# Optimization experiments

Measured on AMD Instinct MI355X. Metric: run time of the kernel, lower is better.

The kernel has to match this reference:

```python
import jax, jax.numpy as jnp
import numpy as np

N = 50000      # nodes
E = 800000     # edges (avg degree 16)
D = 128        # in_channels == hidden_channels (required by x*M + x_hat*~M)
OUT = 64       # fc out_channels


def _linear_params(key, out_f, in_f):
    # torch.nn.Linear default init: U(-1/sqrt(in), 1/sqrt(in))
    bound = 1.0 / np.sqrt(in_f)
    kw, kb = jax.random.split(key)
    W = jax.random.uniform(kw, (out_f, in_f), jnp.float32, -bound, bound)
    b = jax.random.uniform(kb, (out_f,), jnp.float32, -bound, bound)
    return W, b


def setup_inputs() -> dict:
    key = jax.random.key(0)
    ks = jax.random.split(key, 8)
    x = jax.random.normal(ks[0], (N, D), jnp.float32)
    edge_index = jax.random.randint(ks[1], (2, E), 0, N, dtype=jnp.int64)
    edge_weight = jax.random.uniform(ks[2], (E,), jnp.float32)
    M = jax.random.randint(ks[3], (N, D), 0, 2) > 0  # bool mask
    W1, b1 = _linear_params(ks[4], D, D)
    W2, b2 = _linear_params(ks[5], D, D)
    W3, b3 = _linear_params(ks[6], D, D)
    Wf, bf = _linear_params(ks[7], OUT, D)
    # extra Parameter `bias` in each FPLayer is zero-initialized
    z = jnp.zeros((D,), jnp.float32)
    return {"edge_index": edge_index, "edge_weight": edge_weight, "x": x, "M": M,
            "W1": W1, "b1": b1, "bias1": z, "W2": W2, "b2": b2, "bias2": z,
            "W3": W3, "b3": b3, "bias3": z, "Wf": Wf, "bf": bf}


def reference(edge_index, edge_weight, x, M,
              W1, b1, bias1, W2, b2, bias2, W3, b3, bias3, Wf, bf):
    row, col = edge_index[0], edge_index[1]
    n = x.shape[0]
    # symmetric degree normalization based on destination-node in-degree
    deg = jax.ops.segment_sum(jnp.ones(row.shape[0], x.dtype), col, num_segments=n)
    safe = jnp.where(deg > 0, deg, 1.0)
    dinv = jnp.where(deg > 0, 1.0 / jnp.sqrt(safe), 0.0)
    norm = dinv[row] * dinv[col]  # [E]  (edge_weight is unused by message())

    def fp_layer(x_tilde, W, b, bias):
        msg = norm[:, None] * x_tilde[row]                      # [E, D] gather
        agg = jax.ops.segment_sum(msg, col, num_segments=n)     # [N, D] scatter-add
        return agg @ W.T + b + bias

    # conv1: x_hat = 0 -> x_tilde = x*M
    h = jax.nn.relu(fp_layer(jnp.where(M, x, 0.0), W1, b1, bias1))
    h = jax.nn.relu(fp_layer(jnp.where(M, x, h), W2, b2, bias2))
    h = jax.nn.relu(fp_layer(jnp.where(M, x, h), W3, b3, bias3))
    return h @ Wf.T + bf
```

## Files before the change

### kernel.cpp

```cpp
#include <hip/hip_runtime.h>

#define DD 128
#define OUTF 64
#define SCAP 64
#define NBUCK 8
#define PB_CAP 224
#define CHB 96

typedef __attribute__((ext_vector_type(8))) _Float16 fp16x8;
typedef __attribute__((ext_vector_type(8))) unsigned short ushort8;
typedef __attribute__((ext_vector_type(4))) float floatx4;

union h16 { _Float16 f; unsigned short u; };

__global__ __launch_bounds__(256) void setup_kernel(
    const int* __restrict__ ei, unsigned long long* __restrict__ pairbuf,
    int* __restrict__ pcnt, int* __restrict__ cursor, int E, int n,
    const float* __restrict__ x, const void* __restrict__ M,
    _Float16* __restrict__ xsel, int nd4,
    const float* __restrict__ W1, const float* __restrict__ W2,
    const float* __restrict__ W3, const float* __restrict__ Wf,
    _Float16* __restrict__ Bh1, _Float16* __restrict__ Bl1,
    _Float16* __restrict__ Bh2, _Float16* __restrict__ Bl2,
    _Float16* __restrict__ Bh3, _Float16* __restrict__ Bl3,
    _Float16* __restrict__ Bhf, _Float16* __restrict__ Blf,
    int nbA, int nbXt) {
    int bid = blockIdx.x;
    int t = threadIdx.x;
    if (bid < nbA) {
        __shared__ int lcnt[NBUCK];
        __shared__ int s_any;
        for (int z = bid * 256 + t; z < n; z += nbA * 256) cursor[z] = 0;
        if (t < NBUCK) lcnt[t] = 0;
        if (t == 0) s_any = 0;
        __syncthreads();
        int e0 = bid * 1024;
        int es = min(e0 + t * 4, E - 1);
        if (ei[2 * es + 1] != 0) s_any = 1;
        __syncthreads();
        bool is64 = (s_any == 0);
        float binv = (float)NBUCK / (float)n;
        for (int j = 0; j < 4; j++) {
            int e = e0 + j * 256 + t;
            if (e < E) {
                int r, c;
                if (is64) {
                    const long long* p = (const long long*)ei;
                    r = (int)p[e];
                    c = (int)p[(size_t)E + e];
                } else {
                    r = ei[e];
                    c = ei[E + e];
                }
                r = min(max(r, 0), n - 1);
                c = min(max(c, 0), n - 1);
                int b = min(NBUCK - 1, (int)((float)c * binv));
                int pos = atomicAdd(&lcnt[b], 1);
                if (pos < PB_CAP)
                    pairbuf[((size_t)bid * NBUCK + b) * PB_CAP + pos] =
                        ((unsigned long long)(unsigned)c << 32) | (unsigned)r;
            }
        }
        __syncthreads();
        if (t < NBUCK) pcnt[bid * NBUCK + t] = min(lcnt[t], PB_CAP);
    } else if (bid < nbA + nbXt) {
        __shared__ int s_u8;
        if (t == 0) s_u8 = 0;
        __syncthreads();
        int i40 = (bid - nbA) * 256;
        size_t nd = (size_t)nd4 * 4;
        size_t ps = (size_t)i40 * 4 + (size_t)t * 4 + 1;
        if (ps >= nd) ps = nd - 1;
        if (((const unsigned char*)M)[ps] != 0) s_u8 = 1;
        __syncthreads();
        int isU8 = s_u8;
        int i4 = i40 + t;
        if (i4 < nd4) {
            size_t base = (size_t)i4 * 4;
            const float4 xv = *(const float4*)&x[base];
            int m0, m1, m2, m3;
            if (isU8) {
                const unsigned char* mp = (const unsigned char*)M + base;
                m0 = mp[0]; m1 = mp[1]; m2 = mp[2]; m3 = mp[3];
            } else {
                const int* mp = (const int*)M + base;
                m0 = mp[0]; m1 = mp[1]; m2 = mp[2]; m3 = mp[3];
            }
            h16 h0, h1, h2, h3;
            h0.f = (_Float16)xv.x; h1.f = (_Float16)xv.y;
            h2.f = (_Float16)xv.z; h3.f = (_Float16)xv.w;
            unsigned short s0 = m0 ? h0.u : (unsigned short)0xFFFF;
            unsigned short s1 = m1 ? h1.u : (unsigned short)0xFFFF;
            unsigned short s2 = m2 ? h2.u : (unsigned short)0xFFFF;
            unsigned short s3 = m3 ? h3.u : (unsigned short)0xFFFF;
            unsigned long long pk = (unsigned long long)s0 | ((unsigned long long)s1 << 16)
                                  | ((unsigned long long)s2 << 32) | ((unsigned long long)s3 << 48);
            *(unsigned long long*)&xsel[base] = pk;
        }
    } else {
        int tid = (bid - nbA - nbXt) * 256 + t;
        const float* W; _Float16 *Bh, *Bl; int NT, lt;
        if      (tid < 2048) { W = W1; Bh = Bh1; Bl = Bl1; NT = 8; lt = tid; }
        else if (tid < 4096) { W = W2; Bh = Bh2; Bl = Bl2; NT = 8; lt = tid - 2048; }
        else if (tid < 6144) { W = W3; Bh = Bh3; Bl = Bl3; NT = 8; lt = tid - 4096; }
        else if (tid < 7168) { W = Wf; Bh = Bhf; Bl = Blf; NT = 4; lt = tid - 6144; }
        else return;
        int lane = lt & 63;
        int g = lt >> 6;
        int nt = g % NT;
        int chunk = g / NT;
        int o = nt * 16 + (lane & 15);
        int k = chunk * 32 + (lane >> 4) * 8;
        const float* src = W + o * 128 + k;
#pragma unroll
        for (int j = 0; j < 8; j++) {
            float a = src[j];
            _Float16 h = (_Float16)a;
            Bh[(size_t)lt * 8 + j] = h;
            Bl[(size_t)lt * 8 + j] = (_Float16)(a - (float)h);
        }
    }
}

__global__ __launch_bounds__(256) void scatter_kernel(
    const unsigned long long* __restrict__ pairbuf,
    const int* __restrict__ pcnt,
    int* __restrict__ cursor, int* __restrict__ slot, int nbA) {
    int b = blockIdx.x & (NBUCK - 1);
    int chunk = blockIdx.x >> 3;
    int t = threadIdx.x;
    for (int i = chunk; i < nbA; i += CHB) {
        int cnt = pcnt[i * NBUCK + b];
        const unsigned long long* pp = pairbuf + ((size_t)i * NBUCK + b) * PB_CAP;
        for (int j = t; j < cnt; j += 256) {
            unsigned long long pr = pp[j];
            int c = (int)(pr >> 32);
            int r = (int)(unsigned)pr;
            int pos = atomicAdd(&cursor[c], 1);
            if (pos < SCAP)
                slot[(size_t)c * SCAP + pos] = r;
        }
    }
}

template <int SENT>
__global__ __launch_bounds__(256) void agg_kernel(const _Float16* __restrict__ xin,
                                                  const int* __restrict__ cursor,
                                                  const int* __restrict__ slot,
                                                  _Float16* __restrict__ A, int n) {
    int wave = (blockIdx.x * 256 + threadIdx.x) >> 6;
    if (wave >= n) return;
    int lane = threadIdx.x & 63;
    int sid = lane >> 4;
    int li = lane & 15;
    int craw = cursor[wave];
    int cnt = min(craw, SCAP);
    float dc = craw > 0 ? rsqrtf((float)craw) : 0.0f;
    const int* sl = slot + (size_t)wave * SCAP;
    float acc[8] = {0.f, 0.f, 0.f, 0.f, 0.f, 0.f, 0.f, 0.f};
    for (int k = 0; k < cnt; k += 16) {
        int i0 = k + sid;
        int i1 = k + 4 + sid;
        int i2 = k + 8 + sid;
        int i3 = k + 12 + sid;
        int r0 = sl[min(i0, cnt - 1)];
        int r1 = sl[min(i1, cnt - 1)];
        int r2 = sl[min(i2, cnt - 1)];
        int r3 = sl[min(i3, cnt - 1)];
        int c0 = cursor[r0], c1 = cursor[r1], c2 = cursor[r2], c3 = cursor[r3];
        float w0 = (i0 < cnt && c0 > 0) ? dc * rsqrtf((float)c0) : 0.0f;
        float w1 = (i1 < cnt && c1 > 0) ? dc * rsqrtf((float)c1) : 0.0f;
        float w2 = (i2 < cnt && c2 > 0) ? dc * rsqrtf((float)c2) : 0.0f;
        float w3 = (i3 < cnt && c3 > 0) ? dc * rsqrtf((float)c3) : 0.0f;
        ushort8 u0 = *(const ushort8*)&xin[(size_t)r0 * DD + li * 8];
        ushort8 u1 = *(const ushort8*)&xin[(size_t)r1 * DD + li * 8];
        ushort8 u2 = *(const ushort8*)&xin[(size_t)r2 * DD + li * 8];
        ushort8 u3 = *(const ushort8*)&xin[(size_t)r3 * DD + li * 8];
#pragma unroll
        for (int j = 0; j < 8; j++) {
            h16 t0, t1, t2, t3;
            if (SENT) {
                t0.u = (u0[j] == (unsigned short)0xFFFF) ? (unsigned short)0 : u0[j];
                t1.u = (u1[j] == (unsigned short)0xFFFF) ? (unsigned short)0 : u1[j];
                t2.u = (u2[j] == (unsigned short)0xFFFF) ? (unsigned short)0 : u2[j];
                t3.u = (u3[j] == (unsigned short)0xFFFF) ? (unsigned short)0 : u3[j];
            } else {
                t0.u = u0[j]; t1.u = u1[j]; t2.u = u2[j]; t3.u = u3[j];
            }
            acc[j] += w0 * (float)t0.f + w1 * (float)t1.f
                    + w2 * (float)t2.f + w3 * (float)t3.f;
        }
    }
#pragma unroll
    for (int j = 0; j < 8; j++) {
        acc[j] += __shfl_xor(acc[j], 16);
        acc[j] += __shfl_xor(acc[j], 32);
    }
    if (sid == 0) {
        fp16x8 o;
#pragma unroll
        for (int j = 0; j < 8; j++) o[j] = (_Float16)acc[j];
        *(fp16x8*)&A[(size_t)wave * DD + li * 8] = o;
    }
}

template <int MODE>
__global__ __launch_bounds__(256) void gemm_mfma(const _Float16* __restrict__ A,
                                                 const _Float16* __restrict__ Bh,
                                                 const _Float16* __restrict__ Bl,
                                                 const float* __restrict__ b,
                                                 const float* __restrict__ bias,
                                                 const _Float16* __restrict__ B2h,
                                                 const _Float16* __restrict__ B2l,
                                                 const float* __restrict__ b2,
                                                 float* __restrict__ out_f,
                                                 const _Float16* __restrict__ xsel,
                                                 _Float16* __restrict__ xt_out,
                                                 int n) {
    __shared__ __align__(16) _Float16 sh[4][16][136];
    int wid = (blockIdx.x * 256 + threadIdx.x) >> 6;
    int nwaves = n >> 4;
    if (wid >= nwaves) return;
    int n0 = wid * 16;
    int lane = threadIdx.x & 63;
    int li = lane & 15;
    int quad = lane >> 4;
    int wv = (threadIdx.x >> 6) & 3;

    floatx4 acc[8];
#pragma unroll
    for (int nt = 0; nt < 8; nt++)
        acc[nt] = (floatx4){0.f, 0.f, 0.f, 0.f};

    const _Float16* arow = A + (size_t)(n0 + li) * DD + quad * 8;
#pragma unroll
    for (int chunk = 0; chunk < 4; chunk++) {
        fp16x8 a = *(const fp16x8*)(arow + chunk * 32);
#pragma unroll
        for (int nt = 0; nt < 8; nt++) {
            size_t boff = (size_t)(((chunk * 8 + nt) << 6) + lane) * 8;
            fp16x8 b_h = *(const fp16x8*)&Bh[boff];
            fp16x8 b_l = *(const fp16x8*)&Bl[boff];
            acc[nt] = __builtin_amdgcn_mfma_f32_16x16x32_f16(a, b_h, acc[nt], 0, 0, 0);
            acc[nt] = __builtin_amdgcn_mfma_f32_16x16x32_f16(a, b_l, acc[nt], 0, 0, 0);
        }
    }

#pragma unroll
    for (int nt = 0; nt < 8; nt++) {
        int o = nt * 16 + li;
        float bb = b[o] + bias[o];
#pragma unroll
        for (int reg = 0; reg < 4; reg++) {
            float v = fmaxf(acc[nt][reg] + bb, 0.0f);
            sh[wv][quad * 4 + reg][o] = (_Float16)v;
        }
    }
    __asm__ volatile("s_waitcnt lgkmcnt(0)" ::: "memory");

    if (MODE == 0) {
#pragma unroll
        for (int it = 0; it < 4; it++) {
            int node = it * 4 + quad;
            size_t ix = (size_t)(n0 + node) * DD + li * 8;
            fp16x8 hv = *(const fp16x8*)&sh[wv][node][li * 8];
            fp16x8 xv = *(const fp16x8*)&xsel[ix];
            ushort8 xb = *(const ushort8*)&xsel[ix];
            fp16x8 o;
#pragma unroll
            for (int j = 0; j < 8; j++)
                o[j] = (xb[j] == (unsigned short)0xFFFF) ? hv[j] : xv[j];
            *(fp16x8*)&xt_out[ix] = o;
        }
    } else {
        floatx4 acc2[4];
#pragma unroll
        for (int nt = 0; nt < 4; nt++)
            acc2[nt] = (floatx4){0.f, 0.f, 0.f, 0.f};
#pragma unroll
        for (int chunk = 0; chunk < 4; chunk++) {
            fp16x8 a2 = *(const fp16x8*)&sh[wv][li][chunk * 32 + quad * 8];
#pragma unroll
            for (int nt = 0; nt < 4; nt++) {
                size_t boff = (size_t)(((chunk * 4 + nt) << 6) + lane) * 8;
                fp16x8 b_h = *(const fp16x8*)&B2h[boff];
                fp16x8 b_l = *(const fp16x8*)&B2l[boff];
                acc2[nt] = __builtin_amdgcn_mfma_f32_16x16x32_f16(a2, b_h, acc2[nt], 0, 0, 0);
                acc2[nt] = __builtin_amdgcn_mfma_f32_16x16x32_f16(a2, b_l, acc2[nt], 0, 0, 0);
            }
        }
        __asm__ volatile("s_waitcnt lgkmcnt(0)" ::: "memory");
        float* shf = (float*)&sh[wv][0][0];
#pragma unroll
        for (int nt = 0; nt < 4; nt++) {
            int o = nt * 16 + li;
            float bb = b2[o];
#pragma unroll
            for (int reg = 0; reg < 4; reg++)
                shf[(quad * 4 + reg) * 68 + o] = acc2[nt][reg] + bb;
        }
        __asm__ volatile("s_waitcnt lgkmcnt(0)" ::: "memory");
#pragma unroll
        for (int it = 0; it < 4; it++) {
            int node = it * 4 + quad;
            float4 v = *(const float4*)&shf[node * 68 + li * 4];
            *(float4*)&out_f[(size_t)(n0 + node) * OUTF + li * 4] = v;
        }
    }
}

extern "C" void kernel_launch(void* const* d_in, const int* in_sizes, int n_in,
                              void* d_out, int out_size, void* d_ws, size_t ws_size,
                              hipStream_t stream) {
    const int*   ei    = (const int*)d_in[0];
    const float* x     = (const float*)d_in[2];
    const void*  M     = d_in[3];
    const float* W1    = (const float*)d_in[4];
    const float* b1    = (const float*)d_in[5];
    const float* bias1 = (const float*)d_in[6];
    const float* W2    = (const float*)d_in[7];
    const float* b2    = (const float*)d_in[8];
    const float* bias2 = (const float*)d_in[9];
    const float* W3    = (const float*)d_in[10];
    const float* b3    = (const float*)d_in[11];
    const float* bias3 = (const float*)d_in[12];
    const float* Wf    = (const float*)d_in[13];
    const float* bf    = (const float*)d_in[14];

    const int E = in_sizes[1];
    const int N = in_sizes[2] / DD;
    const int ND = N * DD;

    char* w = (char*)d_ws;
    size_t off = 0;
    auto alloc = [&](size_t bytes) -> char* {
        char* p = w + off;
        off = (off + bytes + 255) & ~(size_t)255;
        return p;
    };
    const int nbA = (E + 1023) / 1024;
    int*   cursor = (int*)  alloc((size_t)N * 4);
    int*   slot   = (int*)  alloc((size_t)N * SCAP * 4);
    unsigned long long* pairbuf =
        (unsigned long long*)alloc((size_t)nbA * NBUCK * PB_CAP * 8);
    int*   pcnt   = (int*)  alloc((size_t)nbA * NBUCK * 4);
    _Float16* xsel = (_Float16*)alloc((size_t)ND * 2);
    _Float16* xt   = (_Float16*)alloc((size_t)ND * 2);
    _Float16* Aa   = (_Float16*)alloc((size_t)ND * 2);
    _Float16* Bh1 = (_Float16*)alloc(128 * 128 * 2);
    _Float16* Bl1 = (_Float16*)alloc(128 * 128 * 2);
    _Float16* Bh2 = (_Float16*)alloc(128 * 128 * 2);
    _Float16* Bl2 = (_Float16*)alloc(128 * 128 * 2);
    _Float16* Bh3 = (_Float16*)alloc(128 * 128 * 2);
    _Float16* Bl3 = (_Float16*)alloc(128 * 128 * 2);
    _Float16* Bhf = (_Float16*)alloc(64 * 128 * 2);
    _Float16* Blf = (_Float16*)alloc(64 * 128 * 2);
    (void)ws_size;

    const int nd4 = ND / 4;
    const int nbXt = (nd4 + 255) / 256;
    const int nbPk = 28;

    setup_kernel<<<nbA + nbXt + nbPk, 256, 0, stream>>>(
        ei, pairbuf, pcnt, cursor, E, N,
        x, M, xsel, nd4,
        W1, W2, W3, Wf,
        Bh1, Bl1, Bh2, Bl2, Bh3, Bl3, Bhf, Blf,
        nbA, nbXt);
    scatter_kernel<<<NBUCK * CHB, 256, 0, stream>>>(pairbuf, pcnt, cursor, slot, nbA);

    int nwaves = N / 16;
    int gGrid = (nwaves * 64 + 255) / 256;
    int aggGrid = (N * 64 + 255) / 256;

    agg_kernel<1><<<aggGrid, 256, 0, stream>>>(xsel, cursor, slot, Aa, N);
    gemm_mfma<0><<<gGrid, 256, 0, stream>>>(Aa, Bh1, Bl1, b1, bias1,
                                            nullptr, nullptr, nullptr, nullptr,
                                            xsel, xt, N);
    agg_kernel<0><<<aggGrid, 256, 0, stream>>>(xt, cursor, slot, Aa, N);
    gemm_mfma<0><<<gGrid, 256, 0, stream>>>(Aa, Bh2, Bl2, b2, bias2,
                                            nullptr, nullptr, nullptr, nullptr,
                                            xsel, xt, N);
    agg_kernel<0><<<aggGrid, 256, 0, stream>>>(xt, cursor, slot, Aa, N);
    gemm_mfma<1><<<gGrid, 256, 0, stream>>>(Aa, Bh3, Bl3, b3, bias3,
                                            Bhf, Blf, bf, (float*)d_out,
                                            nullptr, nullptr, N);
}
```

Measured before the change: 292.4 us.

## Prescale node features by source dinv and drop per-edge degree lookups

The symmetric normalization is factored so each node's features are pre-multiplied by its own dinv, both when the masked input is built and in the GEMM epilogue. Aggregation then sums unweighted neighbor rows and applies the destination dinv once, which removes the per-edge cursor gather and rsqrt. The x/M packing moves from the setup kernel into the scatter kernel, and those blocks spin on an atomic counter until the scatter blocks have finished computing degrees. The spin-wait depends on all scatter blocks being resident or scheduled ahead of the waiting blocks, and the prescaling slightly changes where fp16 rounding occurs.

```diff
diff --git a/kernel.cpp b/kernel.cpp
--- a/kernel.cpp
+++ b/kernel.cpp
@@ -6,6 +6,7 @@
 #define NBUCK 8
 #define PB_CAP 224
 #define CHB 96
+#define SCATB (NBUCK * CHB)
 
 typedef __attribute__((ext_vector_type(8))) _Float16 fp16x8;
 typedef __attribute__((ext_vector_type(8))) unsigned short ushort8;
@@ -15,21 +16,21 @@
 
 __global__ __launch_bounds__(256) void setup_kernel(
     const int* __restrict__ ei, unsigned long long* __restrict__ pairbuf,
-    int* __restrict__ pcnt, int* __restrict__ cursor, int E, int n,
-    const float* __restrict__ x, const void* __restrict__ M,
-    _Float16* __restrict__ xsel, int nd4,
+    int* __restrict__ pcnt, int* __restrict__ cursor, int* __restrict__ ctrl,
+    int E, int n,
     const float* __restrict__ W1, const float* __restrict__ W2,
     const float* __restrict__ W3, const float* __restrict__ Wf,
     _Float16* __restrict__ Bh1, _Float16* __restrict__ Bl1,
     _Float16* __restrict__ Bh2, _Float16* __restrict__ Bl2,
     _Float16* __restrict__ Bh3, _Float16* __restrict__ Bl3,
     _Float16* __restrict__ Bhf, _Float16* __restrict__ Blf,
-    int nbA, int nbXt) {
+    int nbA) {
     int bid = blockIdx.x;
     int t = threadIdx.x;
     if (bid < nbA) {
         __shared__ int lcnt[NBUCK];
         __shared__ int s_any;
+        if (bid == 0 && t == 0) ctrl[0] = 0;
         for (int z = bid * 256 + t; z < n; z += nbA * 256) cursor[z] = 0;
         if (t < NBUCK) lcnt[t] = 0;
         if (t == 0) s_any = 0;
@@ -63,42 +64,8 @@
         }
         __syncthreads();
         if (t < NBUCK) pcnt[bid * NBUCK + t] = min(lcnt[t], PB_CAP);
-    } else if (bid < nbA + nbXt) {
-        __shared__ int s_u8;
-        if (t == 0) s_u8 = 0;
-        __syncthreads();
-        int i40 = (bid - nbA) * 256;
-        size_t nd = (size_t)nd4 * 4;
-        size_t ps = (size_t)i40 * 4 + (size_t)t * 4 + 1;
-        if (ps >= nd) ps = nd - 1;
-        if (((const unsigned char*)M)[ps] != 0) s_u8 = 1;
-        __syncthreads();
-        int isU8 = s_u8;
-        int i4 = i40 + t;
-        if (i4 < nd4) {
-            size_t base = (size_t)i4 * 4;
-            const float4 xv = *(const float4*)&x[base];
-            int m0, m1, m2, m3;
-            if (isU8) {
-                const unsigned char* mp = (const unsigned char*)M + base;
-                m0 = mp[0]; m1 = mp[1]; m2 = mp[2]; m3 = mp[3];
-            } else {
-                const int* mp = (const int*)M + base;
-                m0 = mp[0]; m1 = mp[1]; m2 = mp[2]; m3 = mp[3];
-            }
-            h16 h0, h1, h2, h3;
-            h0.f = (_Float16)xv.x; h1.f = (_Float16)xv.y;
-            h2.f = (_Float16)xv.z; h3.f = (_Float16)xv.w;
-            unsigned short s0 = m0 ? h0.u : (unsigned short)0xFFFF;
-            unsigned short s1 = m1 ? h1.u : (unsigned short)0xFFFF;
-            unsigned short s2 = m2 ? h2.u : (unsigned short)0xFFFF;
-            unsigned short s3 = m3 ? h3.u : (unsigned short)0xFFFF;
-            unsigned long long pk = (unsigned long long)s0 | ((unsigned long long)s1 << 16)
-                                  | ((unsigned long long)s2 << 32) | ((unsigned long long)s3 << 48);
-            *(unsigned long long*)&xsel[base] = pk;
-        }
     } else {
-        int tid = (bid - nbA - nbXt) * 256 + t;
+        int tid = (bid - nbA) * 256 + t;
         const float* W; _Float16 *Bh, *Bl; int NT, lt;
         if      (tid < 2048) { W = W1; Bh = Bh1; Bl = Bl1; NT = 8; lt = tid; }
         else if (tid < 4096) { W = W2; Bh = Bh2; Bl = Bl2; NT = 8; lt = tid - 2048; }
@@ -125,20 +92,78 @@
 __global__ __launch_bounds__(256) void scatter_kernel(
     const unsigned long long* __restrict__ pairbuf,
     const int* __restrict__ pcnt,
-    int* __restrict__ cursor, int* __restrict__ slot, int nbA) {
-    int b = blockIdx.x & (NBUCK - 1);
-    int chunk = blockIdx.x >> 3;
+    int* __restrict__ cursor, int* __restrict__ slot, int* __restrict__ ctrl,
+    const float* __restrict__ x, const void* __restrict__ Mv,
+    _Float16* __restrict__ xs0, float* __restrict__ dinv,
+    int nbA, int ndTot) {
+    int bid = blockIdx.x;
     int t = threadIdx.x;
-    for (int i = chunk; i < nbA; i += CHB) {
-        int cnt = pcnt[i * NBUCK + b];
-        const unsigned long long* pp = pairbuf + ((size_t)i * NBUCK + b) * PB_CAP;
-        for (int j = t; j < cnt; j += 256) {
-            unsigned long long pr = pp[j];
-            int c = (int)(pr >> 32);
-            int r = (int)(unsigned)pr;
-            int pos = atomicAdd(&cursor[c], 1);
-            if (pos < SCAP)
-                slot[(size_t)c * SCAP + pos] = r;
+    if (bid < SCATB) {
+        int b = bid & (NBUCK - 1);
+        int chunk = bid >> 3;
+        for (int i = chunk; i < nbA; i += CHB) {
+            int cnt = pcnt[i * NBUCK + b];
+            const unsigned long long* pp = pairbuf + ((size_t)i * NBUCK + b) * PB_CAP;
+            for (int j = t; j < cnt; j += 256) {
+                unsigned long long pr = pp[j];
+                int c = (int)(pr >> 32);
+                int r = (int)(unsigned)pr;
+                int pos = atomicAdd(&cursor[c], 1);
+                if (pos < SCAP)
+                    slot[(size_t)c * SCAP + pos] = r;
+            }
+        }
+        __syncthreads();
+        __threadfence();
+        if (t == 0)
+            __hip_atomic_fetch_add(ctrl, 1, __ATOMIC_RELEASE, __HIP_MEMORY_SCOPE_AGENT);
+    } else {
+        size_t idx = (size_t)(bid - SCATB) * 2048 + (size_t)t * 8;
+        bool act = (idx + 8 <= (size_t)ndTot);
+        float4 xa = {0.f, 0.f, 0.f, 0.f}, xb = {0.f, 0.f, 0.f, 0.f};
+        if (act) {
+            xa = *(const float4*)&x[idx];
+            xb = *(const float4*)&x[idx + 4];
+        }
+        __shared__ int s_u8;
+        if (t == 0) s_u8 = 0;
+        __syncthreads();
+        size_t ps = idx + 1;
+        if (ps >= (size_t)ndTot) ps = (size_t)ndTot - 1;
+        if (((const unsigned char*)Mv)[ps] != 0) s_u8 = 1;
+        __syncthreads();
+        int m[8] = {0, 0, 0, 0, 0, 0, 0, 0};
+        if (act) {
+            if (s_u8) {
+                const unsigned char* mp = (const unsigned char*)Mv + idx;
+#pragma unroll
+                for (int j = 0; j < 8; j++) m[j] = mp[j];
+            } else {
+                const int* mp = (const int*)Mv + idx;
+#pragma unroll
+                for (int j = 0; j < 8; j++) m[j] = mp[j];
+            }
+        }
+        if (t == 0) {
+            while (__hip_atomic_load(ctrl, __ATOMIC_ACQUIRE, __HIP_MEMORY_SCOPE_AGENT) < SCATB)
+                __builtin_amdgcn_s_sleep(2);
+        }
+        __syncthreads();
+        if (act) {
+            int node = (int)(idx >> 7);
+            int deg = __hip_atomic_load(&cursor[node], __ATOMIC_RELAXED,
+                                        __HIP_MEMORY_SCOPE_AGENT);
+            float dv = deg > 0 ? rsqrtf((float)deg) : 0.0f;
+            if ((idx & 127) == 0) dinv[node] = dv;
+            float xf[8] = {xa.x, xa.y, xa.z, xa.w, xb.x, xb.y, xb.z, xb.w};
+            ushort8 o;
+#pragma unroll
+            for (int j = 0; j < 8; j++) {
+                h16 h;
+                h.f = (_Float16)(dv * xf[j]);
+                o[j] = m[j] ? h.u : (unsigned short)0xFFFF;
+            }
+            *(ushort8*)&xs0[idx] = o;
         }
     }
 }
@@ -147,15 +172,15 @@
 __global__ __launch_bounds__(256) void agg_kernel(const _Float16* __restrict__ xin,
                                                   const int* __restrict__ cursor,
                                                   const int* __restrict__ slot,
+                                                  const float* __restrict__ dinv,
                                                   _Float16* __restrict__ A, int n) {
     int wave = (blockIdx.x * 256 + threadIdx.x) >> 6;
     if (wave >= n) return;
     int lane = threadIdx.x & 63;
     int sid = lane >> 4;
     int li = lane & 15;
-    int craw = cursor[wave];
-    int cnt = min(craw, SCAP);
-    float dc = craw > 0 ? rsqrtf((float)craw) : 0.0f;
+    int cnt = min(cursor[wave], SCAP);
+    float dc = dinv[wave];
     const int* sl = slot + (size_t)wave * SCAP;
     float acc[8] = {0.f, 0.f, 0.f, 0.f, 0.f, 0.f, 0.f, 0.f};
     for (int k = 0; k < cnt; k += 16) {
@@ -167,28 +192,35 @@
         int r1 = sl[min(i1, cnt - 1)];
         int r2 = sl[min(i2, cnt - 1)];
         int r3 = sl[min(i3, cnt - 1)];
-        int c0 = cursor[r0], c1 = cursor[r1], c2 = cursor[r2], c3 = cursor[r3];
-        float w0 = (i0 < cnt && c0 > 0) ? dc * rsqrtf((float)c0) : 0.0f;
-        float w1 = (i1 < cnt && c1 > 0) ? dc * rsqrtf((float)c1) : 0.0f;
-        float w2 = (i2 < cnt && c2 > 0) ? dc * rsqrtf((float)c2) : 0.0f;
-        float w3 = (i3 < cnt && c3 > 0) ? dc * rsqrtf((float)c3) : 0.0f;
-        ushort8 u0 = *(const ushort8*)&xin[(size_t)r0 * DD + li * 8];
-        ushort8 u1 = *(const ushort8*)&xin[(size_t)r1 * DD + li * 8];
-        ushort8 u2 = *(const ushort8*)&xin[(size_t)r2 * DD + li * 8];
-        ushort8 u3 = *(const ushort8*)&xin[(size_t)r3 * DD + li * 8];
-#pragma unroll
-        for (int j = 0; j < 8; j++) {
-            h16 t0, t1, t2, t3;
-            if (SENT) {
+        float m0 = i0 < cnt ? 1.0f : 0.0f;
+        float m1 = i1 < cnt ? 1.0f : 0.0f;
+        float m2 = i2 < cnt ? 1.0f : 0.0f;
+        float m3 = i3 < cnt ? 1.0f : 0.0f;
+        if (SENT) {
+            ushort8 u0 = *(const ushort8*)&xin[(size_t)r0 * DD + li * 8];
+            ushort8 u1 = *(const ushort8*)&xin[(size_t)r1 * DD + li * 8];
+            ushort8 u2 = *(const ushort8*)&xin[(size_t)r2 * DD + li * 8];
+            ushort8 u3 = *(const ushort8*)&xin[(size_t)r3 * DD + li * 8];
+#pragma unroll
+            for (int j = 0; j < 8; j++) {
+                h16 t0, t1, t2, t3;
                 t0.u = (u0[j] == (unsigned short)0xFFFF) ? (unsigned short)0 : u0[j];
                 t1.u = (u1[j] == (unsigned short)0xFFFF) ? (unsigned short)0 : u1[j];
                 t2.u = (u2[j] == (unsigned short)0xFFFF) ? (unsigned short)0 : u2[j];
                 t3.u = (u3[j] == (unsigned short)0xFFFF) ? (unsigned short)0 : u3[j];
-            } else {
-                t0.u = u0[j]; t1.u = u1[j]; t2.u = u2[j]; t3.u = u3[j];
-            }
-            acc[j] += w0 * (float)t0.f + w1 * (float)t1.f
-                    + w2 * (float)t2.f + w3 * (float)t3.f;
+                acc[j] += m0 * (float)t0.f + m1 * (float)t1.f
+                        + m2 * (float)t2.f + m3 * (float)t3.f;
+            }
+        } else {
+            fp16x8 v0 = *(const fp16x8*)&xin[(size_t)r0 * DD + li * 8];
+            fp16x8 v1 = *(const fp16x8*)&xin[(size_t)r1 * DD + li * 8];
+            fp16x8 v2 = *(const fp16x8*)&xin[(size_t)r2 * DD + li * 8];
+            fp16x8 v3 = *(const fp16x8*)&xin[(size_t)r3 * DD + li * 8];
+#pragma unroll
+            for (int j = 0; j < 8; j++) {
+                acc[j] += m0 * (float)v0[j] + m1 * (float)v1[j]
+                        + m2 * (float)v2[j] + m3 * (float)v3[j];
+            }
         }
     }
 #pragma unroll
@@ -199,7 +231,7 @@
     if (sid == 0) {
         fp16x8 o;
 #pragma unroll
-        for (int j = 0; j < 8; j++) o[j] = (_Float16)acc[j];
+        for (int j = 0; j < 8; j++) o[j] = (_Float16)(dc * acc[j]);
         *(fp16x8*)&A[(size_t)wave * DD + li * 8] = o;
     }
 }
@@ -210,11 +242,12 @@
                                                  const _Float16* __restrict__ Bl,
                                                  const float* __restrict__ b,
                                                  const float* __restrict__ bias,
+                                                 const float* __restrict__ dinv,
                                                  const _Float16* __restrict__ B2h,
                                                  const _Float16* __restrict__ B2l,
                                                  const float* __restrict__ b2,
                                                  float* __restrict__ out_f,
-                                                 const _Float16* __restrict__ xsel,
+                                                 const _Float16* __restrict__ xs0,
                                                  _Float16* __restrict__ xt_out,
                                                  int n) {
     __shared__ __align__(16) _Float16 sh[4][16][136];
@@ -246,6 +279,11 @@
         }
     }
 
+    float dvr[4] = {1.f, 1.f, 1.f, 1.f};
+    if (MODE == 0) {
+        float4 dv4 = *(const float4*)&dinv[n0 + quad * 4];
+        dvr[0] = dv4.x; dvr[1] = dv4.y; dvr[2] = dv4.z; dvr[3] = dv4.w;
+    }
 #pragma unroll
     for (int nt = 0; nt < 8; nt++) {
         int o = nt * 16 + li;
@@ -253,6 +291,7 @@
 #pragma unroll
         for (int reg = 0; reg < 4; reg++) {
             float v = fmaxf(acc[nt][reg] + bb, 0.0f);
+            if (MODE == 0) v *= dvr[reg];
             sh[wv][quad * 4 + reg][o] = (_Float16)v;
         }
     }
@@ -264,8 +303,8 @@
             int node = it * 4 + quad;
             size_t ix = (size_t)(n0 + node) * DD + li * 8;
             fp16x8 hv = *(const fp16x8*)&sh[wv][node][li * 8];
-            fp16x8 xv = *(const fp16x8*)&xsel[ix];
-            ushort8 xb = *(const ushort8*)&xsel[ix];
+            fp16x8 xv = *(const fp16x8*)&xs0[ix];
+            ushort8 xb = *(const ushort8*)&xs0[ix];
             fp16x8 o;
 #pragma unroll
             for (int j = 0; j < 8; j++)
@@ -339,12 +378,14 @@
         return p;
     };
     const int nbA = (E + 1023) / 1024;
+    int*   ctrl   = (int*)  alloc(256);
     int*   cursor = (int*)  alloc((size_t)N * 4);
     int*   slot   = (int*)  alloc((size_t)N * SCAP * 4);
+    float* dinv   = (float*)alloc((size_t)N * 4);
     unsigned long long* pairbuf =
         (unsigned long long*)alloc((size_t)nbA * NBUCK * PB_CAP * 8);
     int*   pcnt   = (int*)  alloc((size_t)nbA * NBUCK * 4);
-    _Float16* xsel = (_Float16*)alloc((size_t)ND * 2);
+    _Float16* xs0  = (_Float16*)alloc((size_t)ND * 2);
     _Float16* xt   = (_Float16*)alloc((size_t)ND * 2);
     _Float16* Aa   = (_Float16*)alloc((size_t)ND * 2);
     _Float16* Bh1 = (_Float16*)alloc(128 * 128 * 2);
@@ -357,32 +398,31 @@
     _Float16* Blf = (_Float16*)alloc(64 * 128 * 2);
     (void)ws_size;
 
-    const int nd4 = ND / 4;
-    const int nbXt = (nd4 + 255) / 256;
     const int nbPk = 28;
-
-    setup_kernel<<<nbA + nbXt + nbPk, 256, 0, stream>>>(
-        ei, pairbuf, pcnt, cursor, E, N,
-        x, M, xsel, nd4,
+    const int nScale = (ND + 2047) / 2048;
+
+    setup_kernel<<<nbA + nbPk, 256, 0, stream>>>(
+        ei, pairbuf, pcnt, cursor, ctrl, E, N,
         W1, W2, W3, Wf,
         Bh1, Bl1, Bh2, Bl2, Bh3, Bl3, Bhf, Blf,
-        nbA, nbXt);
-    scatter_kernel<<<NBUCK * CHB, 256, 0, stream>>>(pairbuf, pcnt, cursor, slot, nbA);
+        nbA);
+    scatter_kernel<<<SCATB + nScale, 256, 0, stream>>>(
+        pairbuf, pcnt, cursor, slot, ctrl, x, M, xs0, dinv, nbA, ND);
 
     int nwaves = N / 16;
     int gGrid = (nwaves * 64 + 255) / 256;
     int aggGrid = (N * 64 + 255) / 256;
 
-    agg_kernel<1><<<aggGrid, 256, 0, stream>>>(xsel, cursor, slot, Aa, N);
-    gemm_mfma<0><<<gGrid, 256, 0, stream>>>(Aa, Bh1, Bl1, b1, bias1,
+    agg_kernel<1><<<aggGrid, 256, 0, stream>>>(xs0, cursor, slot, dinv, Aa, N);
+    gemm_mfma<0><<<gGrid, 256, 0, stream>>>(Aa, Bh1, Bl1, b1, bias1, dinv,
                                             nullptr, nullptr, nullptr, nullptr,
-                                            xsel, xt, N);
-    agg_kernel<0><<<aggGrid, 256, 0, stream>>>(xt, cursor, slot, Aa, N);
-    gemm_mfma<0><<<gGrid, 256, 0, stream>>>(Aa, Bh2, Bl2, b2, bias2,
+                                            xs0, xt, N);
+    agg_kernel<0><<<aggGrid, 256, 0, stream>>>(xt, cursor, slot, dinv, Aa, N);
+    gemm_mfma<0><<<gGrid, 256, 0, stream>>>(Aa, Bh2, Bl2, b2, bias2, dinv,
                                             nullptr, nullptr, nullptr, nullptr,
-                                            xsel, xt, N);
-    agg_kernel<0><<<aggGrid, 256, 0, stream>>>(xt, cursor, slot, Aa, N);
-    gemm_mfma<1><<<gGrid, 256, 0, stream>>>(Aa, Bh3, Bl3, b3, bias3,
+                                            xs0, xt, N);
+    agg_kernel<0><<<aggGrid, 256, 0, stream>>>(xt, cursor, slot, dinv, Aa, N);
+    gemm_mfma<1><<<gGrid, 256, 0, stream>>>(Aa, Bh3, Bl3, b3, bias3, nullptr,
                                             Bhf, Blf, bf, (float*)d_out,
                                             nullptr, nullptr, N);
 }
```

Measured after the change: 668.1 us. 2.28x slower.
